# Optimization experiments

Hardware: AMD Instinct MI355X
Metric: run time of the kernel (lower is better)

## Reference

```python
import jax, jax.numpy as jnp
import numpy as np

TOPK = 2
ALPHA = 0.1
EPS = 1e-20


def setup_inputs() -> dict:
    key = jax.random.key(0)
    k1, k2 = jax.random.split(key)
    hidden_states = jax.random.normal(k1, (4, 4096, 2048), dtype=jnp.float32)
    # kaiming_uniform_(a=sqrt(5)) on [E, H] ~ U(-1/sqrt(H), 1/sqrt(H))
    bound = 1.0 / np.sqrt(2048)
    weight = jax.random.uniform(k2, (64, 2048), dtype=jnp.float32, minval=-bound, maxval=bound)
    return {"hidden_states": hidden_states, "weight": weight}


def reference(hidden_states, weight):
    B, S, H = hidden_states.shape
    E = weight.shape[0]
    x = hidden_states.reshape(-1, H)                      # [B*S, H]
    logits = jnp.einsum('th,eh->te', x, weight)           # [B*S, E]
    scores = jax.nn.softmax(logits, axis=-1)
    topk_weight, topk_idx = jax.lax.top_k(scores, TOPK)   # [B*S, K]
    # norm_topk_prob
    topk_weight = topk_weight / (topk_weight.sum(axis=-1, keepdims=True) + EPS)
    # seq_aux load-balancing loss (training path)
    idx = topk_idx.reshape(B, S * TOPK)                   # [B, S*K]
    ce = jnp.zeros((B, E), dtype=scores.dtype)
    ce = ce.at[jnp.arange(B)[:, None], idx].add(1.0)      # scatter_add counts
    ce = ce * (E / (S * TOPK))
    expert_scores = scores.reshape(B, S, E).mean(axis=1)  # [B, E]
    aux_loss = (ce * expert_scores).sum(axis=1).mean() * ALPHA
    return topk_idx, topk_weight, aux_loss
```

## Files before the change

### kernel.cpp

```cpp
#include <hip/hip_runtime.h>

#define TAU 8e-3f

typedef __attribute__((ext_vector_type(8))) short bf16x8;
typedef __attribute__((ext_vector_type(4))) float f32x4;
typedef __attribute__((ext_vector_type(4))) unsigned int u32x4;

#define PS_OFF 262144
#define PC_OFF (262144 + 262144)

#define RNE16(f) \
  ((unsigned short)((__float_as_uint(f) + 0x7fffu + ((__float_as_uint(f) >> 16) & 1u)) >> 16))

#define CVTPK(dst, a, b) \
  asm("v_cvt_pk_bf16_f32 %0, %1, %2" : "=v"(dst) : "v"(a), "v"(b))

#define GL16(gp, lp)                                                          \
  __builtin_amdgcn_global_load_lds(                                           \
      (const __attribute__((address_space(1))) unsigned int*)(gp),            \
      (__attribute__((address_space(3))) unsigned int*)(lp), 16, 0, 0)

__global__ __launch_bounds__(256) void wconv(const float* __restrict__ W,
                                             unsigned short* __restrict__ Wswz) {
  int t = blockIdx.x * 256 + threadIdx.x;
  int g = t >> 12, rem = t & 4095;
  int ks = rem >> 6, lane = rem & 63;
  int fm = lane & 15, kg = lane >> 4;
  const float* src = W + (size_t)(g * 16 + fm) * 2048 + ks * 32 + kg * 8;
  float4 a = *(const float4*)src;
  float4 b = *(const float4*)(src + 4);
  ushort4 lo = make_ushort4(RNE16(a.x), RNE16(a.y), RNE16(a.z), RNE16(a.w));
  ushort4 hi = make_ushort4(RNE16(b.x), RNE16(b.y), RNE16(b.z), RNE16(b.w));
  unsigned short* dst = Wswz + (size_t)t * 8;
  *(ushort4*)dst = lo;
  *(ushort4*)(dst + 4) = hi;
}

__global__ __launch_bounds__(256, 4) void gate_fused(
    const float* __restrict__ x, const float* __restrict__ Wf,
    const unsigned short* __restrict__ Wswz,
    float* __restrict__ out, float* __restrict__ ps, float* __restrict__ pc) {
  __shared__ float __attribute__((aligned(16))) xlds[2][2048];
  __shared__ float part[16][68];
  __shared__ float sm[4][64];
  __shared__ float cn[4][64];

  const int tid = threadIdx.x;
  const int lane = tid & 63;
  const int w = __builtin_amdgcn_readfirstlane(tid >> 6);
  const int fm = lane & 15;
  const int kg = lane >> 4;
  const int tok0 = blockIdx.x * 16;

  const float* src0;
  const float* src1;
  {
    int p0 = tid, q0 = p0 ^ ((p0 >> 5) & 7);
    int p1 = 256 + tid, q1 = p1 ^ ((p1 >> 5) & 7);
    src0 = x + (size_t)(tok0 + (q0 >> 5)) * 2048 + (q0 & 31) * 4;
    src1 = x + (size_t)(tok0 + (q1 >> 5)) * 2048 + (q1 & 31) * 4;
  }
  float* lds_d0 = &xlds[0][tid * 4];
  float* lds_d1 = &xlds[0][1024 + tid * 4];

  const char* lb0 = (const char*)xlds + fm * 512 + (((kg * 2 + 0) ^ (fm & 7)) * 16);
  const char* lb1 = (const char*)xlds + fm * 512 + (((kg * 2 + 1) ^ (fm & 7)) * 16);

  const bf16x8* wsw = (const bf16x8*)Wswz + lane;

  f32x4 acc = (f32x4){0.f, 0.f, 0.f, 0.f};

#define STEP(BUF, S, DO_STAGE)                                               \
  {                                                                          \
    bf16x8 b0 = wsw[(w * 64 + (S) * 4 + 0) * 64];                            \
    bf16x8 b1 = wsw[(w * 64 + (S) * 4 + 1) * 64];                            \
    bf16x8 b2 = wsw[(w * 64 + (S) * 4 + 2) * 64];                            \
    bf16x8 b3 = wsw[(w * 64 + (S) * 4 + 3) * 64];                            \
    if (DO_STAGE) {                                                          \
      GL16(src0 + ((S) + 1) * 128, lds_d0 + (1 - (BUF)) * 2048);             \
      GL16(src1 + ((S) + 1) * 128, lds_d1 + (1 - (BUF)) * 2048);             \
    }                                                                        \
    _Pragma("unroll")                                                        \
    for (int ks = 0; ks < 4; ++ks) {                                         \
      float4 lo = *(const float4*)(lb0 + (BUF)*8192 + ks * 128);             \
      float4 hi = *(const float4*)(lb1 + (BUF)*8192 + ks * 128);             \
      unsigned u0, u1, u2, u3;                                               \
      CVTPK(u0, lo.x, lo.y);                                                 \
      CVTPK(u1, lo.z, lo.w);                                                 \
      CVTPK(u2, hi.x, hi.y);                                                 \
      CVTPK(u3, hi.z, hi.w);                                                 \
      u32x4 uu = (u32x4){u0, u1, u2, u3};                                    \
      bf16x8 a = __builtin_bit_cast(bf16x8, uu);                             \
      bf16x8 bb = (ks == 0) ? b0 : (ks == 1) ? b1 : (ks == 2) ? b2 : b3;     \
      acc = __builtin_amdgcn_mfma_f32_16x16x32_bf16(a, bb, acc, 0, 0, 0);    \
    }                                                                        \
    __syncthreads();                                                         \
  }

  GL16(src0, lds_d0);
  GL16(src1, lds_d1);
  __syncthreads();

#pragma unroll 1
  for (int s = 0; s < 14; s += 2) {
    STEP(0, s, true)
    STEP(1, s + 1, true)
  }
  STEP(0, 14, true)
  STEP(1, 15, false)
#undef STEP

#pragma unroll
  for (int r = 0; r < 4; ++r) part[kg * 4 + r][w * 16 + fm] = acc[r];
  __syncthreads();

  float ssum = 0.f;
  float cnt = 0.f;

  for (int i = 0; i < 4; ++i) {
    const int tl = w * 4 + i;
    const int tok = tok0 + tl;
    float v = part[tl][lane];

    float m1 = v; int i1 = lane;
#pragma unroll
    for (int o = 32; o; o >>= 1) {
      float ov = __shfl_xor(m1, o, 64);
      int oi = __shfl_xor(i1, o, 64);
      if (ov > m1 || (ov == m1 && oi < i1)) { m1 = ov; i1 = oi; }
    }
    float v2 = (lane == i1) ? -3e38f : v;
    float m2 = v2; int i2 = lane;
#pragma unroll
    for (int o = 32; o; o >>= 1) {
      float ov = __shfl_xor(m2, o, 64);
      int oi = __shfl_xor(i2, o, 64);
      if (ov > m2 || (ov == m2 && oi < i2)) { m2 = ov; i2 = oi; }
    }
    float m3 = (lane == i1 || lane == i2) ? -3e38f : v;
#pragma unroll
    for (int o = 32; o; o >>= 1) m3 = fmaxf(m3, __shfl_xor(m3, o, 64));

    if ((m1 - m2 < TAU) || (m2 - m3 < TAU)) {
      unsigned long long cand = __ballot(v >= m2 - TAU);
      const float* xr2 = x + (size_t)tok * 2048 + lane * 32;
      while (cand) {
        int e = __ffsll(cand) - 1;
        cand &= cand - 1;
        const float* wr = Wf + (size_t)e * 2048 + lane * 32;
        float s = 0.f;
#pragma unroll
        for (int kk = 0; kk < 32; kk += 8) {
          float4 u0 = *(const float4*)(xr2 + kk);
          float4 w0 = *(const float4*)(wr + kk);
          float4 u1 = *(const float4*)(xr2 + kk + 4);
          float4 w1 = *(const float4*)(wr + kk + 4);
          s += u0.x * w0.x + u0.y * w0.y + u0.z * w0.z + u0.w * w0.w +
               u1.x * w1.x + u1.y * w1.y + u1.z * w1.z + u1.w * w1.w;
        }
#pragma unroll
        for (int o = 32; o; o >>= 1) s += __shfl_xor(s, o, 64);
        if (lane == e) v = s;
      }
      m1 = v; i1 = lane;
#pragma unroll
      for (int o = 32; o; o >>= 1) {
        float ov = __shfl_xor(m1, o, 64);
        int oi = __shfl_xor(i1, o, 64);
        if (ov > m1 || (ov == m1 && oi < i1)) { m1 = ov; i1 = oi; }
      }
      v2 = (lane == i1) ? -3e38f : v;
      m2 = v2; i2 = lane;
#pragma unroll
      for (int o = 32; o; o >>= 1) {
        float ov = __shfl_xor(m2, o, 64);
        int oi = __shfl_xor(i2, o, 64);
        if (ov > m2 || (ov == m2 && oi < i2)) { m2 = ov; i2 = oi; }
      }
    }

    float ez = __expf(v - m1);
    float Z = ez;
#pragma unroll
    for (int o = 32; o; o >>= 1) Z += __shfl_xor(Z, o, 64);
    float iz = 1.f / Z;
    float p1 = iz;
    float p2 = __expf(m2 - m1) * iz;
    float dn = 1.f / (p1 + p2 + 1e-20f);
    if (lane == 0) {
      size_t tg = (size_t)tok;
      out[tg * 2 + 0] = (float)i1;
      out[tg * 2 + 1] = (float)i2;
      out[32768 + tg * 2 + 0] = p1 * dn;
      out[32768 + tg * 2 + 1] = p2 * dn;
    }
    ssum += ez * iz;
    cnt += (float)((lane == i1) + (lane == i2));
  }

  sm[w][lane] = ssum;
  cn[w][lane] = cnt;
  __syncthreads();

  if (tid < 64) {
    float s = 0.f, c = 0.f;
#pragma unroll
    for (int ww = 0; ww < 4; ++ww) { s += sm[ww][tid]; c += cn[ww][tid]; }
    ps[(size_t)blockIdx.x * 64 + tid] = s;
    pc[(size_t)blockIdx.x * 64 + tid] = c;
  }
}

__global__ __launch_bounds__(1024) void aux_final(
    const float* __restrict__ ps, const float* __restrict__ pc,
    float* __restrict__ out) {
  __shared__ float rs[1024], rc[1024];
  const int tid = threadIdx.x;
  const int e = tid & 63;
  const int b = (tid >> 6) & 3;
  const int q = tid >> 8;

  float s = 0.f, c = 0.f;
#pragma unroll 8
  for (int i = 0; i < 64; ++i) {
    int blk = b * 256 + q * 64 + i;
    s += ps[(size_t)blk * 64 + e];
    c += pc[(size_t)blk * 64 + e];
  }
  rs[tid] = s;
  rc[tid] = c;
  __syncthreads();

  if (tid < 256) {
    float ss = rs[tid] + rs[256 + tid] + rs[512 + tid] + rs[768 + tid];
    float cc = rc[tid] + rc[256 + tid] + rc[512 + tid] + rc[768 + tid];
    rs[tid] = cc * (1.f / 128.f) * (ss * (1.f / 4096.f));
  }
  __syncthreads();
  if (tid < 64) {
    float tot = rs[tid] + rs[64 + tid] + rs[128 + tid] + rs[192 + tid];
#pragma unroll
    for (int o = 32; o; o >>= 1) tot += __shfl_xor(tot, o, 64);
    if (tid == 0) out[65536] = 0.025f * tot;
  }
}

extern "C" void kernel_launch(void* const* d_in, const int* in_sizes, int n_in,
                              void* d_out, int out_size, void* d_ws, size_t ws_size,
                              hipStream_t stream) {
  const float* x = (const float*)d_in[0];
  const float* Wf = (const float*)d_in[1];
  float* out = (float*)d_out;
  unsigned short* Wswz = (unsigned short*)d_ws;
  float* ps = (float*)((char*)d_ws + PS_OFF);
  float* pc = (float*)((char*)d_ws + PC_OFF);
  wconv<<<64, 256, 0, stream>>>(Wf, Wswz);
  gate_fused<<<1024, 256, 0, stream>>>(x, Wf, Wswz, out, ps, pc);
  aux_final<<<1, 1024, 0, stream>>>(ps, pc, out);
}
```

Before: 214.6 us.

## Triple-buffer x staging with prefetch distance two and explicit vmcnt waits

Moves the LDS staging of x from a double buffer to a triple buffer, issuing global-to-LDS loads two K-steps ahead. It waits with explicit s_waitcnt vmcnt counts and raw barriers instead of full __syncthreads, and fully unrolls the 16 steps. The aim is to hide more global load latency in this memory-bound GEMV-like gate. In exchange it uses more LDS, which may reduce occupancy, and it relies on hand-counted vmcnt values that must also cover the W loads issued in each step.

Result: no change. 214.9 us (+0.2%).

```diff
diff --git a/kernel.cpp b/kernel.cpp
--- a/kernel.cpp
+++ b/kernel.cpp
@@ -40,7 +40,7 @@
     const float* __restrict__ x, const float* __restrict__ Wf,
     const unsigned short* __restrict__ Wswz,
     float* __restrict__ out, float* __restrict__ ps, float* __restrict__ pc) {
-  __shared__ float __attribute__((aligned(16))) xlds[2][2048];
+  __shared__ float __attribute__((aligned(16))) xlds[3][2048];
   __shared__ float part[16][68];
   __shared__ float sm[4][64];
   __shared__ float cn[4][64];
@@ -70,20 +70,22 @@
 
   f32x4 acc = (f32x4){0.f, 0.f, 0.f, 0.f};
 
-#define STEP(BUF, S, DO_STAGE)                                               \
+#define KSTEP(S, VW, DO_STAGE)                                               \
   {                                                                          \
+    if (DO_STAGE) {                                                          \
+      GL16(src0 + ((S) + 2) * 128, lds_d0 + (((S) + 2) % 3) * 2048);         \
+      GL16(src1 + ((S) + 2) * 128, lds_d1 + (((S) + 2) % 3) * 2048);         \
+    }                                                                        \
+    asm volatile("s_waitcnt vmcnt(" #VW ")" ::: "memory");                   \
+    __builtin_amdgcn_s_barrier();                                            \
     bf16x8 b0 = wsw[(w * 64 + (S) * 4 + 0) * 64];                            \
     bf16x8 b1 = wsw[(w * 64 + (S) * 4 + 1) * 64];                            \
     bf16x8 b2 = wsw[(w * 64 + (S) * 4 + 2) * 64];                            \
     bf16x8 b3 = wsw[(w * 64 + (S) * 4 + 3) * 64];                            \
-    if (DO_STAGE) {                                                          \
-      GL16(src0 + ((S) + 1) * 128, lds_d0 + (1 - (BUF)) * 2048);             \
-      GL16(src1 + ((S) + 1) * 128, lds_d1 + (1 - (BUF)) * 2048);             \
-    }                                                                        \
     _Pragma("unroll")                                                        \
     for (int ks = 0; ks < 4; ++ks) {                                         \
-      float4 lo = *(const float4*)(lb0 + (BUF)*8192 + ks * 128);             \
-      float4 hi = *(const float4*)(lb1 + (BUF)*8192 + ks * 128);             \
+      float4 lo = *(const float4*)(lb0 + ((S) % 3) * 8192 + ks * 128);       \
+      float4 hi = *(const float4*)(lb1 + ((S) % 3) * 8192 + ks * 128);       \
       unsigned u0, u1, u2, u3;                                               \
       CVTPK(u0, lo.x, lo.y);                                                 \
       CVTPK(u1, lo.z, lo.w);                                                 \
@@ -94,21 +96,19 @@
       bf16x8 bb = (ks == 0) ? b0 : (ks == 1) ? b1 : (ks == 2) ? b2 : b3;     \
       acc = __builtin_amdgcn_mfma_f32_16x16x32_bf16(a, bb, acc, 0, 0, 0);    \
     }                                                                        \
-    __syncthreads();                                                         \
+    __builtin_amdgcn_s_barrier();                                            \
   }
 
   GL16(src0, lds_d0);
   GL16(src1, lds_d1);
-  __syncthreads();
-
-#pragma unroll 1
-  for (int s = 0; s < 14; s += 2) {
-    STEP(0, s, true)
-    STEP(1, s + 1, true)
-  }
-  STEP(0, 14, true)
-  STEP(1, 15, false)
-#undef STEP
+  GL16(src0 + 128, lds_d0 + 2048);
+  GL16(src1 + 128, lds_d1 + 2048);
+
+  KSTEP(0, 4, 1)  KSTEP(1, 4, 1)  KSTEP(2, 4, 1)  KSTEP(3, 4, 1)
+  KSTEP(4, 4, 1)  KSTEP(5, 4, 1)  KSTEP(6, 4, 1)  KSTEP(7, 4, 1)
+  KSTEP(8, 4, 1)  KSTEP(9, 4, 1)  KSTEP(10, 4, 1) KSTEP(11, 4, 1)
+  KSTEP(12, 4, 1) KSTEP(13, 4, 1) KSTEP(14, 2, 0) KSTEP(15, 0, 0)
+#undef KSTEP
 
 #pragma unroll
   for (int r = 0; r < 4; ++r) part[kg * 4 + r][w * 16 + fm] = acc[r];
```
